# Optimization experiments

Hardware: AMD Instinct MI355X
Metric: run time of the kernel (lower is better)

## Reference

```python
import jax, jax.numpy as jnp
import numpy as np

N_NODES = 100000
N_EDGES = 1600000
IN_FEATURES = 128
OUT_FEATURES = 32


def setup_inputs() -> dict:
    key = jax.random.key(0)
    k_x, k_w, k_r, k_c, k_v = jax.random.split(key, 5)
    x = jax.random.normal(k_x, (N_NODES, IN_FEATURES), dtype=jnp.float32)
    # One fused (in_features, out_features) weight == concat of the out_features Dense(in,1) layers
    W = jax.random.normal(k_w, (IN_FEATURES, OUT_FEATURES), dtype=jnp.float32) / np.sqrt(IN_FEATURES)
    b = jnp.zeros((OUT_FEATURES,), dtype=jnp.float32)
    edge_rows = jax.random.randint(k_r, (N_EDGES,), 0, N_NODES, dtype=jnp.int64)
    edge_cols = jax.random.randint(k_c, (N_EDGES,), 0, N_NODES, dtype=jnp.int64)
    edge_vals = jax.random.uniform(k_v, (N_EDGES,), dtype=jnp.float32)
    return {"x": x, "W": W, "b": b, "edge_rows": edge_rows,
            "edge_cols": edge_cols, "edge_vals": edge_vals}


def reference(x, W, b, edge_rows, edge_cols, edge_vals):
    # z_i = dense_i(x) for all i at once: (N, out_features)
    z = x @ W + b
    # per nonzero edge e=(r,c) with adjacency value w_e:
    #   (z*adj).values + (z^T*adj).values = w_e * (z[r] + z[c])   -> (E, out_features)
    out = edge_vals[:, None] * (z[edge_rows] + z[edge_cols])
    return out
```

## Files before the change

### kernel.cpp

```cpp
#include <hip/hip_runtime.h>

#define NODES 100000
#define IN_F 128
#define OUT_F 32

__global__ __launch_bounds__(256) void zgemm_kernel(
    const float* __restrict__ x, const float* __restrict__ W,
    const float* __restrict__ b, float* __restrict__ z, int n_nodes)
{
    __shared__ float xs[64 * IN_F];
    __shared__ float Ws[IN_F * OUT_F];
    __shared__ float bs[OUT_F];

    const int t = threadIdx.x;
    const int row0 = blockIdx.x * 64;
    const int rows = min(64, n_nodes - row0);

    {
        const float4* Wv = (const float4*)W;
        float4* Wsv = (float4*)Ws;
        #pragma unroll
        for (int i = 0; i < 4; ++i)
            Wsv[t + i * 256] = Wv[t + i * 256];
        if (t < OUT_F) bs[t] = b[t];
    }
    {
        const float4* xv = (const float4*)(x + (size_t)row0 * IN_F);
        float4* xsv = (float4*)xs;
        const int nv = rows * (IN_F / 4);
        for (int i = t; i < nv; i += 256)
            xsv[i] = xv[i];
    }
    __syncthreads();

    const int col = t & 31;
    const int rg  = t >> 5;

    float acc[8];
    #pragma unroll
    for (int i = 0; i < 8; ++i) acc[i] = 0.f;

    for (int k = 0; k < IN_F; ++k) {
        const float wv = Ws[k * OUT_F + col];
        #pragma unroll
        for (int i = 0; i < 8; ++i)
            acc[i] += xs[(rg + i * 8) * IN_F + k] * wv;
    }

    const float bb = bs[col];
    #pragma unroll
    for (int i = 0; i < 8; ++i) {
        const int r = rg + i * 8;
        if (r < rows)
            z[(size_t)(row0 + r) * OUT_F + col] = acc[i] + bb;
    }
}

__global__ __launch_bounds__(256) void edge_kernel(
    const int* __restrict__ erows, const int* __restrict__ ecols,
    const float* __restrict__ evals, const float* __restrict__ z,
    float* __restrict__ out, int n_edges)
{
    const size_t g = (size_t)blockIdx.x * 256 + threadIdx.x;
    const size_t e = g >> 3;
    if (e >= (size_t)n_edges) return;
    const int joff = (int)(g & 7) << 2;

    const int r = erows[e];
    const int c = ecols[e];
    const float w = evals[e];

    const float4 zr = *(const float4*)(z + (size_t)r * OUT_F + joff);
    const float4 zc = *(const float4*)(z + (size_t)c * OUT_F + joff);

    float4 o;
    o.x = w * (zr.x + zc.x);
    o.y = w * (zr.y + zc.y);
    o.z = w * (zr.z + zc.z);
    o.w = w * (zr.w + zc.w);

    *(float4*)(out + e * OUT_F + joff) = o;
}

extern "C" void kernel_launch(void* const* d_in, const int* in_sizes, int n_in,
                              void* d_out, int out_size, void* d_ws, size_t ws_size,
                              hipStream_t stream)
{
    const float* x  = (const float*)d_in[0];
    const float* W  = (const float*)d_in[1];
    const float* b  = (const float*)d_in[2];
    const int* erow = (const int*)d_in[3];
    const int* ecol = (const int*)d_in[4];
    const float* ev = (const float*)d_in[5];

    const int n_nodes = in_sizes[0] / IN_F;
    const int n_edges = in_sizes[3];

    float* z   = (float*)d_ws;
    float* out = (float*)d_out;

    const int gemm_blocks = (n_nodes + 63) / 64;
    zgemm_kernel<<<gemm_blocks, 256, 0, stream>>>(x, W, b, z, n_nodes);

    const size_t total_thr = (size_t)n_edges * 8;
    const int edge_blocks = (int)((total_thr + 255) / 256);
    edge_kernel<<<edge_blocks, 256, 0, stream>>>(erow, ecol, ev, z, out, n_edges);
}
```

Before: 328.1 us.

## Store intermediate z in bf16, restructure GEMM mapping, use nontemporal edge I/O

The GEMM now stores z as packed bf16, which halves the size of the intermediate table that the edge kernel gathers twice per edge. The GEMM thread mapping is also reworked: each thread owns one row and 8 output columns, reads x from padded shared memory as float4, and reads W straight from global memory. The edge kernel unpacks the bf16 values, and uses nontemporal loads for the edge arrays and nontemporal stores for the output. Rounding z to bf16 loses precision and may push results past tolerance.

```diff
diff --git a/kernel.cpp b/kernel.cpp
--- a/kernel.cpp
+++ b/kernel.cpp
@@ -1,85 +1,100 @@
 #include <hip/hip_runtime.h>
 
-#define NODES 100000
 #define IN_F 128
 #define OUT_F 32
+#define XS_STRIDE 132
+
+typedef float  vfloat4 __attribute__((ext_vector_type(4)));
+
+__device__ __forceinline__ unsigned int pack_bf16x2(float a, float b) {
+    unsigned int ua = __float_as_uint(a);
+    unsigned int ub = __float_as_uint(b);
+    ua = (ua + 0x7FFFu + ((ua >> 16) & 1u)) >> 16;
+    ub = (ub + 0x7FFFu + ((ub >> 16) & 1u)) & 0xFFFF0000u;
+    return ua | ub;
+}
 
 __global__ __launch_bounds__(256) void zgemm_kernel(
     const float* __restrict__ x, const float* __restrict__ W,
-    const float* __restrict__ b, float* __restrict__ z, int n_nodes)
+    const float* __restrict__ b, unsigned int* __restrict__ zb, int n_nodes)
 {
-    __shared__ float xs[64 * IN_F];
-    __shared__ float Ws[IN_F * OUT_F];
-    __shared__ float bs[OUT_F];
+    __shared__ float xs[64 * XS_STRIDE];
 
     const int t = threadIdx.x;
     const int row0 = blockIdx.x * 64;
     const int rows = min(64, n_nodes - row0);
 
     {
-        const float4* Wv = (const float4*)W;
-        float4* Wsv = (float4*)Ws;
-        #pragma unroll
-        for (int i = 0; i < 4; ++i)
-            Wsv[t + i * 256] = Wv[t + i * 256];
-        if (t < OUT_F) bs[t] = b[t];
-    }
-    {
         const float4* xv = (const float4*)(x + (size_t)row0 * IN_F);
-        float4* xsv = (float4*)xs;
         const int nv = rows * (IN_F / 4);
-        for (int i = t; i < nv; i += 256)
-            xsv[i] = xv[i];
+        for (int i = t; i < nv; i += 256) {
+            const int r  = i >> 5;
+            const int c4 = i & 31;
+            *(float4*)&xs[r * XS_STRIDE + c4 * 4] = xv[i];
+        }
     }
     __syncthreads();
 
-    const int col = t & 31;
-    const int rg  = t >> 5;
+    const int row = t & 63;
+    const int cg  = t >> 6;
+    const float* __restrict__ Wc = W + cg * 8;
 
     float acc[8];
     #pragma unroll
-    for (int i = 0; i < 8; ++i) acc[i] = 0.f;
+    for (int c = 0; c < 8; ++c) acc[c] = 0.f;
 
-    for (int k = 0; k < IN_F; ++k) {
-        const float wv = Ws[k * OUT_F + col];
+    #pragma unroll 8
+    for (int k4 = 0; k4 < IN_F / 4; ++k4) {
+        const float4 xv = *(const float4*)&xs[row * XS_STRIDE + k4 * 4];
+        const float xk[4] = {xv.x, xv.y, xv.z, xv.w};
         #pragma unroll
-        for (int i = 0; i < 8; ++i)
-            acc[i] += xs[(rg + i * 8) * IN_F + k] * wv;
+        for (int kk = 0; kk < 4; ++kk) {
+            const int k = k4 * 4 + kk;
+            #pragma unroll
+            for (int c = 0; c < 8; ++c)
+                acc[c] = fmaf(xk[kk], Wc[k * OUT_F + c], acc[c]);
+        }
     }
 
-    const float bb = bs[col];
-    #pragma unroll
-    for (int i = 0; i < 8; ++i) {
-        const int r = rg + i * 8;
-        if (r < rows)
-            z[(size_t)(row0 + r) * OUT_F + col] = acc[i] + bb;
+    if (row < rows) {
+        const float* __restrict__ bc = b + cg * 8;
+        float v[8];
+        #pragma unroll
+        for (int c = 0; c < 8; ++c) v[c] = acc[c] + bc[c];
+        uint4 o;
+        o.x = pack_bf16x2(v[0], v[1]);
+        o.y = pack_bf16x2(v[2], v[3]);
+        o.z = pack_bf16x2(v[4], v[5]);
+        o.w = pack_bf16x2(v[6], v[7]);
+        *(uint4*)(zb + (size_t)(row0 + row) * 16 + cg * 4) = o;
     }
 }
 
 __global__ __launch_bounds__(256) void edge_kernel(
     const int* __restrict__ erows, const int* __restrict__ ecols,
-    const float* __restrict__ evals, const float* __restrict__ z,
+    const float* __restrict__ evals, const unsigned int* __restrict__ zb,
     float* __restrict__ out, int n_edges)
 {
     const size_t g = (size_t)blockIdx.x * 256 + threadIdx.x;
     const size_t e = g >> 3;
     if (e >= (size_t)n_edges) return;
-    const int joff = (int)(g & 7) << 2;
+    const int l8 = (int)(g & 7);
 
-    const int r = erows[e];
-    const int c = ecols[e];
-    const float w = evals[e];
+    const int   r = __builtin_nontemporal_load(erows + e);
+    const int   c = __builtin_nontemporal_load(ecols + e);
+    const float w = __builtin_nontemporal_load(evals + e);
 
-    const float4 zr = *(const float4*)(z + (size_t)r * OUT_F + joff);
-    const float4 zc = *(const float4*)(z + (size_t)c * OUT_F + joff);
+    const uint2 ur = *(const uint2*)(zb + (size_t)r * 16 + l8 * 2);
+    const uint2 uc = *(const uint2*)(zb + (size_t)c * 16 + l8 * 2);
 
-    float4 o;
-    o.x = w * (zr.x + zc.x);
-    o.y = w * (zr.y + zc.y);
-    o.z = w * (zr.z + zc.z);
-    o.w = w * (zr.w + zc.w);
+    vfloat4 o;
+    o.x = w * (__uint_as_float(ur.x << 16)         + __uint_as_float(uc.x << 16));
+    o.y = w * (__uint_as_float(ur.x & 0xFFFF0000u) + __uint_as_float(uc.x & 0xFFFF0000u));
+    o.z = w * (__uint_as_float(ur.y << 16)         + __uint_as_float(uc.y << 16));
+    o.w = w * (__uint_as_float(ur.y & 0xFFFF0000u) + __uint_as_float(uc.y & 0xFFFF0000u));
 
-    *(float4*)(out + e * OUT_F + joff) = o;
+    vfloat4* dst = (vfloat4*)(out + e * OUT_F + l8 * 4);
+    __builtin_nontemporal_store(o, dst);
 }
 
 extern "C" void kernel_launch(void* const* d_in, const int* in_sizes, int n_in,
@@ -96,13 +111,13 @@
     const int n_nodes = in_sizes[0] / IN_F;
     const int n_edges = in_sizes[3];
 
-    float* z   = (float*)d_ws;
+    unsigned int* zb = (unsigned int*)d_ws;
     float* out = (float*)d_out;
 
     const int gemm_blocks = (n_nodes + 63) / 64;
-    zgemm_kernel<<<gemm_blocks, 256, 0, stream>>>(x, W, b, z, n_nodes);
+    zgemm_kernel<<<gemm_blocks, 256, 0, stream>>>(x, W, b, zb, n_nodes);
 
     const size_t total_thr = (size_t)n_edges * 8;
     const int edge_blocks = (int)((total_thr + 255) / 256);
-    edge_kernel<<<edge_blocks, 256, 0, stream>>>(erow, ecol, ev, z, out, n_edges);
+    edge_kernel<<<edge_blocks, 256, 0, stream>>>(erow, ecol, ev, zb, out, n_edges);
 }
```

Result: slower. 346.4 us (+5.6%).
